# Optimization experiments

Measured on AMD Instinct MI355X. Metric: run time of the kernel, lower is better.

Reference implementation:

```python
import jax, jax.numpy as jnp
import numpy as np

N_NODES = 100000
N_EDGES = 1600000
D = 128


def _sage_conv(x, src, dst, W_l, b_l, W_r, num_nodes):
    # gather source-node features along edges, mean-aggregate at destination
    msg_sum = jax.ops.segment_sum(x[src], dst, num_segments=num_nodes)  # [N, D]
    cnt = jax.ops.segment_sum(jnp.ones((src.shape[0], 1), x.dtype), dst,
                              num_segments=num_nodes)                   # [N, 1]
    agg = msg_sum / jnp.maximum(cnt, 1.0)
    # PyG SAGEConv: lin_l(aggregated) + bias + lin_r(self), root linear has no bias
    return agg @ W_l + b_l + x @ W_r


def setup_inputs() -> dict:
    key = jax.random.key(0)
    ks = jax.random.split(key, 8)
    scale = 1.0 / np.sqrt(D)
    x = jax.random.normal(ks[0], (N_NODES, D), dtype=jnp.float32)
    edge_index = jax.random.randint(ks[1], (2, N_EDGES), 0, N_NODES, dtype=jnp.int64)
    W_l1 = jax.random.normal(ks[2], (D, D), dtype=jnp.float32) * scale
    b_l1 = jnp.zeros((D,), dtype=jnp.float32)
    W_r1 = jax.random.normal(ks[3], (D, D), dtype=jnp.float32) * scale
    W_l2 = jax.random.normal(ks[4], (D, D), dtype=jnp.float32) * scale
    b_l2 = jnp.zeros((D,), dtype=jnp.float32)
    W_r2 = jax.random.normal(ks[5], (D, D), dtype=jnp.float32) * scale
    return {"x": x, "edge_index": edge_index, "W_l1": W_l1, "b_l1": b_l1,
            "W_r1": W_r1, "W_l2": W_l2, "b_l2": b_l2, "W_r2": W_r2}


def reference(x, edge_index, W_l1, b_l1, W_r1, W_l2, b_l2, W_r2):
    src, dst = edge_index[0], edge_index[1]
    n = x.shape[0]
    h = jax.nn.relu(_sage_conv(x, src, dst, W_l1, b_l1, W_r1, n))
    out = _sage_conv(h, src, dst, W_l2, b_l2, W_r2, n)
    return out
```

## Files before the change

kernel.cpp:

```cpp
#include <hip/hip_runtime.h>
#include <hip/hip_bf16.h>

#define DF 128
#define BSH 7
#define BNODES (1 << BSH)
#define SRCBITS 17
#define SRCMASK ((1u << SRCBITS) - 1u)
#define NBLK 512
#define SLABSH 13
#define NKEYS (BNODES * 16)

typedef __attribute__((ext_vector_type(8))) short short8;
typedef __attribute__((ext_vector_type(4))) float floatx4;

__device__ __forceinline__ unsigned short f2bf(float f) {
  unsigned u = __float_as_uint(f);
  u += 0x7fffu + ((u >> 16) & 1u);
  return (unsigned short)(u >> 16);
}
__device__ __forceinline__ float bflo(unsigned u) { return __uint_as_float(u << 16); }
__device__ __forceinline__ float bfhi(unsigned u) { return __uint_as_float(u & 0xffff0000u); }


__global__ __launch_bounds__(256) void count_and_conv(const int* __restrict__ dst,
                                                      int* __restrict__ histg,
                                                      int e, int nb, int chunk,
                                                      const float* __restrict__ x,
                                                      unsigned short* __restrict__ xb, int n4) {
  int t = threadIdx.x;
  if (blockIdx.x < NBLK) {
    __shared__ int h[1024];
    int blk = blockIdx.x;
    for (int i = t; i < nb; i += 256) h[i] = 0;
    __syncthreads();
    int s = blk * chunk, en = min(e, s + chunk);
    for (int i = s + t; i < en; i += 256) atomicAdd(&h[dst[i] >> BSH], 1);
    __syncthreads();
    for (int b = t; b < nb; b += 256) histg[blk * nb + b] = h[b];
  } else {
    int i = (blockIdx.x - NBLK) * 256 + t;
    if (i < n4) {
      float4 v = ((const float4*)x)[i];
      union { unsigned short u[4]; uint2 d; } o;
      o.u[0] = f2bf(v.x); o.u[1] = f2bf(v.y); o.u[2] = f2bf(v.z); o.u[3] = f2bf(v.w);
      ((uint2*)xb)[i] = o.d;
    }
  }
}

__global__ __launch_bounds__(256) void scan_and_reorder(int* __restrict__ histg,
                                                        int* __restrict__ tot, int nb, int sb,
                                                        const float* __restrict__ W0,
                                                        const float* __restrict__ W1,
                                                        const float* __restrict__ W2,
                                                        const float* __restrict__ W3,
                                                        unsigned short* __restrict__ wf) {
  if ((int)blockIdx.x < sb) {
    int wave = threadIdx.x >> 6, lane = threadIdx.x & 63;
    int b = blockIdx.x * 4 + wave;
    if (b >= nb) return;
    int v[8];
    int s = 0;
#pragma unroll
    for (int j = 0; j < 8; ++j) {
      v[j] = histg[(lane * 8 + j) * nb + b];
      s += v[j];
    }
    int S = s;
#pragma unroll
    for (int o = 1; o < 64; o <<= 1) {
      int u = __shfl_up(S, o);
      if (lane >= o) S += u;
    }
    int base = S - s;
#pragma unroll
    for (int j = 0; j < 8; ++j) {
      int c = v[j];
      histg[(lane * 8 + j) * nb + b] = base;
      base += c;
    }
    if (lane == 63) tot[b] = S;
  } else {
    int bb = blockIdx.x - sb;
    int m = bb >> 6;
    const float* W = (m == 0) ? W0 : (m == 1) ? W1 : (m == 2) ? W2 : W3;
    int t = (bb & 63) * 256 + threadIdx.x;
    int j = t & 7, lane = (t >> 3) & 63, ktnt = t >> 9;
    int nt = ktnt & 7, kt = ktnt >> 3;
    int k = kt * 32 + (lane >> 4) * 8 + j;
    int ncol = nt * 16 + (lane & 15);
    wf[m * 16384 + t] = f2bf(W[k * DF + ncol]);
  }
}

__global__ __launch_bounds__(1024) void scan_tot(const int* __restrict__ tot,
                                                 int* __restrict__ bko, int nb, int e) {
  __shared__ int wsum[16];
  int t = threadIdx.x;
  int v = (t < nb) ? tot[t] : 0;
  int lane = t & 63, wid = t >> 6;
  int s = v;
#pragma unroll
  for (int off = 1; off < 64; off <<= 1) {
    int u = __shfl_up(s, off);
    if (lane >= off) s += u;
  }
  if (lane == 63) wsum[wid] = s;
  __syncthreads();
  if (wid == 0) {
    int ws = (lane < 16) ? wsum[lane] : 0;
#pragma unroll
    for (int off = 1; off < 16; off <<= 1) {
      int u = __shfl_up(ws, off);
      if (lane >= off) ws += u;
    }
    if (lane < 16) wsum[lane] = ws;
  }
  __syncthreads();
  int incl = s + ((wid > 0) ? wsum[wid - 1] : 0);
  if (t < nb) bko[t] = incl - v;
  if (t == 0) bko[nb] = e;
}

__global__ __launch_bounds__(256) void part_scatter(const int* __restrict__ src,
                                                    const int* __restrict__ dst,
                                                    const int* __restrict__ histg,
                                                    const int* __restrict__ bko,
                                                    unsigned* __restrict__ ebuf,
                                                    int e, int nb, int chunk) {
  __shared__ int cur[1024];
  int t = threadIdx.x, blk = blockIdx.x;
  for (int b = t; b < nb; b += 256) cur[b] = bko[b] + histg[blk * nb + b];
  __syncthreads();
  int s = blk * chunk, en = min(e, s + chunk);
  for (int i = s + t; i < en; i += 256) {
    int d = dst[i];
    int p = atomicAdd(&cur[d >> BSH], 1);
    ebuf[p] = ((unsigned)(d & (BNODES - 1)) << SRCBITS) | (unsigned)src[i];
  }
}

__global__ __launch_bounds__(256) void fill_fine(const unsigned* __restrict__ ebuf,
                                                 const int* __restrict__ bko,
                                                 int* __restrict__ rs,
                                                 int* __restrict__ csr, int n) {
  __shared__ int hist[NKEYS];
  __shared__ int cur[NKEYS];
  __shared__ int wsum[4];
  int b = blockIdx.x;
  int t = threadIdx.x;
  for (int i = t; i < NKEYS; i += 256) hist[i] = 0;
  __syncthreads();
  int s = bko[b], e = bko[b + 1];
  for (int i = s + t; i < e; i += 256) {
    unsigned p = ebuf[i];
    int key = (int)((p >> SRCBITS) << 4) | (int)((p & SRCMASK) >> SLABSH);
    atomicAdd(&hist[key], 1);
  }
  __syncthreads();
  int v[8], sum = 0;
#pragma unroll
  for (int j = 0; j < 8; ++j) { v[j] = hist[t * 8 + j]; sum += v[j]; }
  int lane = t & 63, wid = t >> 6;
  int S = sum;
#pragma unroll
  for (int o = 1; o < 64; o <<= 1) {
    int u = __shfl_up(S, o);
    if (lane >= o) S += u;
  }
  if (lane == 63) wsum[wid] = S;
  __syncthreads();
  if (wid == 0 && lane < 4) {
    int ws = wsum[lane];
#pragma unroll
    for (int o = 1; o < 4; o <<= 1) {
      int u = __shfl_up(ws, o);
      if (lane >= o) ws += u;
    }
    wsum[lane] = ws;
  }
  __syncthreads();
  int base = (S - sum) + ((wid > 0) ? wsum[wid - 1] : 0);
#pragma unroll
  for (int j = 0; j < 8; ++j) { cur[t * 8 + j] = base; base += v[j]; }
  __syncthreads();
  if (t < BNODES) {
    int g = (b << BSH) + t;
    if (g < n) {
      int endoff = (t == BNODES - 1) ? (e - s) : cur[(t + 1) << 4];
      rs[g] = s + endoff;
    }
  }
  __syncthreads();
  for (int i = s + t; i < e; i += 256) {
    unsigned p = ebuf[i];
    int key = (int)((p >> SRCBITS) << 4) | (int)((p & SRCMASK) >> SLABSH);
    int r = atomicAdd(&cur[key], 1);
    csr[s + r] = (int)(p & SRCMASK);
  }
}

__global__ __launch_bounds__(256) void agg_pull(const uint4* __restrict__ feat,
                                                const int* __restrict__ rs,
                                                const int* __restrict__ csr,
                                                uint4* __restrict__ out, int n) {
  int node = (blockIdx.x * 256 + threadIdx.x) >> 4;
  int l = threadIdx.x & 15;
  if (node >= n) return;
  int s = (node > 0) ? rs[node - 1] : 0;
  int e = rs[node];
  float a0 = 0.f, a1 = 0.f, a2 = 0.f, a3 = 0.f;
  float a4 = 0.f, a5 = 0.f, a6 = 0.f, a7 = 0.f;
  int i = s;
  for (; i + 7 < e; i += 8) {
    int idx[8];
#pragma unroll
    for (int k = 0; k < 8; ++k) idx[k] = csr[i + k];
    uint4 u[8];
#pragma unroll
    for (int k = 0; k < 8; ++k) u[k] = feat[idx[k] * 16 + l];
#pragma unroll
    for (int k = 0; k < 8; ++k) {
      a0 += bflo(u[k].x); a1 += bfhi(u[k].x);
      a2 += bflo(u[k].y); a3 += bfhi(u[k].y);
      a4 += bflo(u[k].z); a5 += bfhi(u[k].z);
      a6 += bflo(u[k].w); a7 += bfhi(u[k].w);
    }
  }
  for (; i < e; ++i) {
    uint4 u = feat[csr[i] * 16 + l];
    a0 += bflo(u.x); a1 += bfhi(u.x);
    a2 += bflo(u.y); a3 += bfhi(u.y);
    a4 += bflo(u.z); a5 += bfhi(u.z);
    a6 += bflo(u.w); a7 += bfhi(u.w);
  }
  float sc = 1.0f / (float)max(e - s, 1);
  uint4 o;
  o.x = (unsigned)f2bf(a0 * sc) | ((unsigned)f2bf(a1 * sc) << 16);
  o.y = (unsigned)f2bf(a2 * sc) | ((unsigned)f2bf(a3 * sc) << 16);
  o.z = (unsigned)f2bf(a4 * sc) | ((unsigned)f2bf(a5 * sc) << 16);
  o.w = (unsigned)f2bf(a6 * sc) | ((unsigned)f2bf(a7 * sc) << 16);
  out[node * 16 + l] = o;
}

__global__ __launch_bounds__(256) void gemm_sage(const unsigned short* __restrict__ Aagg,
                                                 const unsigned short* __restrict__ Aself,
                                                 const unsigned short* __restrict__ WFl,
                                                 const unsigned short* __restrict__ WFr,
                                                 const float* __restrict__ bias,
                                                 void* __restrict__ outp, int n,
                                                 int relu_out_bf16) {
  int wave = threadIdx.x >> 6;
  int lane = threadIdx.x & 63;
  int l16 = lane & 15, quad = lane >> 4;
  int rbase = (blockIdx.x * 4 + wave) * 32;
  if (rbase >= n) return;

  floatx4 acc[2][8];
#pragma unroll
  for (int a = 0; a < 2; ++a)
#pragma unroll
    for (int b = 0; b < 8; ++b) acc[a][b] = (floatx4)0.0f;

  int r0 = min(rbase + l16, n - 1);
  int r1 = min(rbase + 16 + l16, n - 1);

#pragma unroll
  for (int s = 0; s < 2; ++s) {
    const unsigned short* A = s ? Aself : Aagg;
    const unsigned short* W = s ? WFr : WFl;
#pragma unroll
    for (int kt = 0; kt < 4; ++kt) {
      short8 a0 = *(const short8*)(A + r0 * DF + kt * 32 + quad * 8);
      short8 a1 = *(const short8*)(A + r1 * DF + kt * 32 + quad * 8);
#pragma unroll
      for (int nt = 0; nt < 8; ++nt) {
        short8 bf = *(const short8*)(W + (((kt * 8 + nt) * 64) + lane) * 8);
        acc[0][nt] = __builtin_amdgcn_mfma_f32_16x16x32_bf16(a0, bf, acc[0][nt], 0, 0, 0);
        acc[1][nt] = __builtin_amdgcn_mfma_f32_16x16x32_bf16(a1, bf, acc[1][nt], 0, 0, 0);
      }
    }
  }

  float bv[8];
#pragma unroll
  for (int nt = 0; nt < 8; ++nt) bv[nt] = bias[nt * 16 + l16];

  if (relu_out_bf16) {
    unsigned short* O = (unsigned short*)outp;
#pragma unroll
    for (int rb = 0; rb < 2; ++rb)
#pragma unroll
      for (int i = 0; i < 4; ++i) {
        int row = rbase + rb * 16 + quad * 4 + i;
        if (row < n) {
#pragma unroll
          for (int nt = 0; nt < 8; ++nt) {
            float v = acc[rb][nt][i] + bv[nt];
            O[row * DF + nt * 16 + l16] = f2bf(fmaxf(v, 0.0f));
          }
        }
      }
  } else {
    float* O = (float*)outp;
#pragma unroll
    for (int rb = 0; rb < 2; ++rb)
#pragma unroll
      for (int i = 0; i < 4; ++i) {
        int row = rbase + rb * 16 + quad * 4 + i;
        if (row < n) {
#pragma unroll
          for (int nt = 0; nt < 8; ++nt)
            O[row * DF + nt * 16 + l16] = acc[rb][nt][i] + bv[nt];
        }
      }
  }
}


extern "C" void kernel_launch(void* const* d_in, const int* in_sizes, int n_in,
                              void* d_out, int out_size, void* d_ws, size_t ws_size,
                              hipStream_t stream) {
  const float* x   = (const float*)d_in[0];
  const int*   ei  = (const int*)d_in[1];
  const float* Wl1 = (const float*)d_in[2];
  const float* bl1 = (const float*)d_in[3];
  const float* Wr1 = (const float*)d_in[4];
  const float* Wl2 = (const float*)d_in[5];
  const float* bl2 = (const float*)d_in[6];
  const float* Wr2 = (const float*)d_in[7];

  int n = in_sizes[0] / DF;
  int e = in_sizes[1] / 2;
  const int* srcv = ei;
  const int* dstv = ei + e;
  int nb = (n + BNODES - 1) >> BSH;
  int chunk = (e + NBLK - 1) / NBLK;

  char* ws = (char*)d_ws;
  size_t off = 0;
  auto alloc = [&](size_t bytes) {
    void* p = ws + off;
    off = (off + bytes + 255) & ~(size_t)255;
    return p;
  };
  int* histg = (int*)alloc((size_t)nb * NBLK * 4);
  int* tot   = (int*)alloc(4096);
  int* bko   = (int*)alloc((size_t)(nb + 1) * 4);
  int* rs    = (int*)alloc((size_t)n * 4);
  unsigned* ebuf = (unsigned*)alloc((size_t)e * 4);
  int* csr   = (int*)alloc((size_t)e * 4);
  unsigned short* xb   = (unsigned short*)alloc((size_t)n * DF * 2);
  unsigned short* hb   = (unsigned short*)alloc((size_t)n * DF * 2);
  unsigned short* aggb = (unsigned short*)alloc((size_t)n * DF * 2);
  unsigned short* wf   = (unsigned short*)alloc(4 * DF * DF * 2);
  unsigned short* wfl1 = wf;
  unsigned short* wfr1 = wf + 16384;
  unsigned short* wfl2 = wf + 32768;
  unsigned short* wfr2 = wf + 49152;

  int n4 = n * DF / 4;
  int cb = (n4 + 255) / 256;
  count_and_conv<<<NBLK + cb, 256, 0, stream>>>(dstv, histg, e, nb, chunk, x, xb, n4);
  int sb = (nb + 3) / 4;
  scan_and_reorder<<<sb + 256, 256, 0, stream>>>(histg, tot, nb, sb,
                                                 Wl1, Wr1, Wl2, Wr2, wf);
  scan_tot<<<1, 1024, 0, stream>>>(tot, bko, nb, e);
  part_scatter<<<NBLK, 256, 0, stream>>>(srcv, dstv, histg, bko, ebuf, e, nb, chunk);
  fill_fine<<<nb, 256, 0, stream>>>(ebuf, bko, rs, csr, n);

  agg_pull<<<(n * 16 + 255) / 256, 256, 0, stream>>>((const uint4*)xb, rs, csr,
                                                     (uint4*)aggb, n);
  gemm_sage<<<(n + 127) / 128, 256, 0, stream>>>(aggb, xb, wfl1, wfr1, bl1, hb, n, 1);
  agg_pull<<<(n * 16 + 255) / 256, 256, 0, stream>>>((const uint4*)hb, rs, csr,
                                                     (uint4*)aggb, n);
  gemm_sage<<<(n + 127) / 128, 256, 0, stream>>>(aggb, hb, wfl2, wfr2, bl2, d_out, n, 0);
}
```

Measured before the change: 361.5 us.

## Fuse neighbor mean-aggregation into SAGE GEMM via swizzled shared-memory tile

Merges the gather/mean aggregation kernel and the MFMA GEMM into one kernel per layer. Each block aggregates 128 nodes into an XOR-swizzled LDS tile, then multiplies that tile by W_l and the self features by W_r. This removes the bf16 aggregate buffer's global write and re-read plus two launches. In exchange each block now does 8 sequential node aggregations per 16-lane group, and the grid shrinks to about 782 blocks, which may lower memory-level parallelism for the latency-bound gather.

```diff
diff --git a/kernel.cpp b/kernel.cpp
--- a/kernel.cpp
+++ b/kernel.cpp
@@ -48,6 +48,7 @@
   }
 }
 
+
 __global__ __launch_bounds__(256) void scan_and_reorder(int* __restrict__ histg,
                                                         int* __restrict__ tot, int nb, int sb,
                                                         const float* __restrict__ W0,
@@ -200,85 +201,102 @@
   }
 }
 
-__global__ __launch_bounds__(256) void agg_pull(const uint4* __restrict__ feat,
-                                                const int* __restrict__ rs,
-                                                const int* __restrict__ csr,
-                                                uint4* __restrict__ out, int n) {
-  int node = (blockIdx.x * 256 + threadIdx.x) >> 4;
-  int l = threadIdx.x & 15;
-  if (node >= n) return;
-  int s = (node > 0) ? rs[node - 1] : 0;
-  int e = rs[node];
-  float a0 = 0.f, a1 = 0.f, a2 = 0.f, a3 = 0.f;
-  float a4 = 0.f, a5 = 0.f, a6 = 0.f, a7 = 0.f;
-  int i = s;
-  for (; i + 7 < e; i += 8) {
-    int idx[8];
-#pragma unroll
-    for (int k = 0; k < 8; ++k) idx[k] = csr[i + k];
-    uint4 u[8];
-#pragma unroll
-    for (int k = 0; k < 8; ++k) u[k] = feat[idx[k] * 16 + l];
-#pragma unroll
-    for (int k = 0; k < 8; ++k) {
-      a0 += bflo(u[k].x); a1 += bfhi(u[k].x);
-      a2 += bflo(u[k].y); a3 += bfhi(u[k].y);
-      a4 += bflo(u[k].z); a5 += bfhi(u[k].z);
-      a6 += bflo(u[k].w); a7 += bfhi(u[k].w);
-    }
-  }
-  for (; i < e; ++i) {
-    uint4 u = feat[csr[i] * 16 + l];
-    a0 += bflo(u.x); a1 += bfhi(u.x);
-    a2 += bflo(u.y); a3 += bfhi(u.y);
-    a4 += bflo(u.z); a5 += bfhi(u.z);
-    a6 += bflo(u.w); a7 += bfhi(u.w);
-  }
-  float sc = 1.0f / (float)max(e - s, 1);
-  uint4 o;
-  o.x = (unsigned)f2bf(a0 * sc) | ((unsigned)f2bf(a1 * sc) << 16);
-  o.y = (unsigned)f2bf(a2 * sc) | ((unsigned)f2bf(a3 * sc) << 16);
-  o.z = (unsigned)f2bf(a4 * sc) | ((unsigned)f2bf(a5 * sc) << 16);
-  o.w = (unsigned)f2bf(a6 * sc) | ((unsigned)f2bf(a7 * sc) << 16);
-  out[node * 16 + l] = o;
-}
-
-__global__ __launch_bounds__(256) void gemm_sage(const unsigned short* __restrict__ Aagg,
-                                                 const unsigned short* __restrict__ Aself,
-                                                 const unsigned short* __restrict__ WFl,
-                                                 const unsigned short* __restrict__ WFr,
-                                                 const float* __restrict__ bias,
-                                                 void* __restrict__ outp, int n,
-                                                 int relu_out_bf16) {
-  int wave = threadIdx.x >> 6;
-  int lane = threadIdx.x & 63;
+__global__ __launch_bounds__(256) void sage_fused(const uint4* __restrict__ feat,
+                                                  const int* __restrict__ rs,
+                                                  const int* __restrict__ csr,
+                                                  const unsigned short* __restrict__ WFl,
+                                                  const unsigned short* __restrict__ WFr,
+                                                  const float* __restrict__ bias,
+                                                  void* __restrict__ outp, int n,
+                                                  int relu_out_bf16) {
+  __shared__ uint4 As[BNODES][16];
+  int t = threadIdx.x;
+  int b = blockIdx.x;
+  int g = t >> 4, l = t & 15;
+
+  for (int j = 0; j < 8; ++j) {
+    int lr = g * 8 + j;
+    int node = (b << BSH) + lr;
+    uint4 o;
+    if (node < n) {
+      int s = (node > 0) ? rs[node - 1] : 0;
+      int e = rs[node];
+      float a0 = 0.f, a1 = 0.f, a2 = 0.f, a3 = 0.f;
+      float a4 = 0.f, a5 = 0.f, a6 = 0.f, a7 = 0.f;
+      int i = s;
+      for (; i + 7 < e; i += 8) {
+        int idx[8];
+#pragma unroll
+        for (int k = 0; k < 8; ++k) idx[k] = csr[i + k];
+        uint4 u[8];
+#pragma unroll
+        for (int k = 0; k < 8; ++k) u[k] = feat[idx[k] * 16 + l];
+#pragma unroll
+        for (int k = 0; k < 8; ++k) {
+          a0 += bflo(u[k].x); a1 += bfhi(u[k].x);
+          a2 += bflo(u[k].y); a3 += bfhi(u[k].y);
+          a4 += bflo(u[k].z); a5 += bfhi(u[k].z);
+          a6 += bflo(u[k].w); a7 += bfhi(u[k].w);
+        }
+      }
+      for (; i < e; ++i) {
+        uint4 u = feat[csr[i] * 16 + l];
+        a0 += bflo(u.x); a1 += bfhi(u.x);
+        a2 += bflo(u.y); a3 += bfhi(u.y);
+        a4 += bflo(u.z); a5 += bfhi(u.z);
+        a6 += bflo(u.w); a7 += bfhi(u.w);
+      }
+      float sc = 1.0f / (float)max(e - s, 1);
+      o.x = (unsigned)f2bf(a0 * sc) | ((unsigned)f2bf(a1 * sc) << 16);
+      o.y = (unsigned)f2bf(a2 * sc) | ((unsigned)f2bf(a3 * sc) << 16);
+      o.z = (unsigned)f2bf(a4 * sc) | ((unsigned)f2bf(a5 * sc) << 16);
+      o.w = (unsigned)f2bf(a6 * sc) | ((unsigned)f2bf(a7 * sc) << 16);
+    } else {
+      o.x = 0u; o.y = 0u; o.z = 0u; o.w = 0u;
+    }
+    As[lr][l ^ (lr & 7)] = o;
+  }
+  __syncthreads();
+
+  int wave = t >> 6;
+  int lane = t & 63;
   int l16 = lane & 15, quad = lane >> 4;
-  int rbase = (blockIdx.x * 4 + wave) * 32;
-  if (rbase >= n) return;
+  int rbase = wave * 32;
+  int grow = (b << BSH) + rbase;
+  if (grow >= n) return;
 
   floatx4 acc[2][8];
 #pragma unroll
   for (int a = 0; a < 2; ++a)
 #pragma unroll
-    for (int b = 0; b < 8; ++b) acc[a][b] = (floatx4)0.0f;
-
-  int r0 = min(rbase + l16, n - 1);
-  int r1 = min(rbase + 16 + l16, n - 1);
-
-#pragma unroll
-  for (int s = 0; s < 2; ++s) {
-    const unsigned short* A = s ? Aself : Aagg;
-    const unsigned short* W = s ? WFr : WFl;
-#pragma unroll
-    for (int kt = 0; kt < 4; ++kt) {
-      short8 a0 = *(const short8*)(A + r0 * DF + kt * 32 + quad * 8);
-      short8 a1 = *(const short8*)(A + r1 * DF + kt * 32 + quad * 8);
-#pragma unroll
-      for (int nt = 0; nt < 8; ++nt) {
-        short8 bf = *(const short8*)(W + (((kt * 8 + nt) * 64) + lane) * 8);
-        acc[0][nt] = __builtin_amdgcn_mfma_f32_16x16x32_bf16(a0, bf, acc[0][nt], 0, 0, 0);
-        acc[1][nt] = __builtin_amdgcn_mfma_f32_16x16x32_bf16(a1, bf, acc[1][nt], 0, 0, 0);
-      }
+    for (int c = 0; c < 8; ++c) acc[a][c] = (floatx4)0.0f;
+
+  int r0l = rbase + l16;
+  int r1l = rbase + 16 + l16;
+  const unsigned short* Asf = (const unsigned short*)feat;
+  int r0g = min(grow + l16, n - 1);
+  int r1g = min(grow + 16 + l16, n - 1);
+
+#pragma unroll
+  for (int kt = 0; kt < 4; ++kt) {
+    short8 a0 = *(const short8*)&As[r0l][(kt * 4 + quad) ^ (r0l & 7)];
+    short8 a1 = *(const short8*)&As[r1l][(kt * 4 + quad) ^ (r1l & 7)];
+#pragma unroll
+    for (int nt = 0; nt < 8; ++nt) {
+      short8 bf = *(const short8*)(WFl + (((kt * 8 + nt) * 64) + lane) * 8);
+      acc[0][nt] = __builtin_amdgcn_mfma_f32_16x16x32_bf16(a0, bf, acc[0][nt], 0, 0, 0);
+      acc[1][nt] = __builtin_amdgcn_mfma_f32_16x16x32_bf16(a1, bf, acc[1][nt], 0, 0, 0);
+    }
+  }
+#pragma unroll
+  for (int kt = 0; kt < 4; ++kt) {
+    short8 a0 = *(const short8*)(Asf + r0g * DF + kt * 32 + quad * 8);
+    short8 a1 = *(const short8*)(Asf + r1g * DF + kt * 32 + quad * 8);
+#pragma unroll
+    for (int nt = 0; nt < 8; ++nt) {
+      short8 bf = *(const short8*)(WFr + (((kt * 8 + nt) * 64) + lane) * 8);
+      acc[0][nt] = __builtin_amdgcn_mfma_f32_16x16x32_bf16(a0, bf, acc[0][nt], 0, 0, 0);
+      acc[1][nt] = __builtin_amdgcn_mfma_f32_16x16x32_bf16(a1, bf, acc[1][nt], 0, 0, 0);
     }
   }
 
@@ -292,7 +310,7 @@
     for (int rb = 0; rb < 2; ++rb)
 #pragma unroll
       for (int i = 0; i < 4; ++i) {
-        int row = rbase + rb * 16 + quad * 4 + i;
+        int row = grow + rb * 16 + quad * 4 + i;
         if (row < n) {
 #pragma unroll
           for (int nt = 0; nt < 8; ++nt) {
@@ -307,7 +325,7 @@
     for (int rb = 0; rb < 2; ++rb)
 #pragma unroll
       for (int i = 0; i < 4; ++i) {
-        int row = rbase + rb * 16 + quad * 4 + i;
+        int row = grow + rb * 16 + quad * 4 + i;
         if (row < n) {
 #pragma unroll
           for (int nt = 0; nt < 8; ++nt)
@@ -352,7 +370,6 @@
   int* csr   = (int*)alloc((size_t)e * 4);
   unsigned short* xb   = (unsigned short*)alloc((size_t)n * DF * 2);
   unsigned short* hb   = (unsigned short*)alloc((size_t)n * DF * 2);
-  unsigned short* aggb = (unsigned short*)alloc((size_t)n * DF * 2);
   unsigned short* wf   = (unsigned short*)alloc(4 * DF * DF * 2);
   unsigned short* wfl1 = wf;
   unsigned short* wfr1 = wf + 16384;
@@ -369,10 +386,6 @@
   part_scatter<<<NBLK, 256, 0, stream>>>(srcv, dstv, histg, bko, ebuf, e, nb, chunk);
   fill_fine<<<nb, 256, 0, stream>>>(ebuf, bko, rs, csr, n);
 
-  agg_pull<<<(n * 16 + 255) / 256, 256, 0, stream>>>((const uint4*)xb, rs, csr,
-                                                     (uint4*)aggb, n);
-  gemm_sage<<<(n + 127) / 128, 256, 0, stream>>>(aggb, xb, wfl1, wfr1, bl1, hb, n, 1);
-  agg_pull<<<(n * 16 + 255) / 256, 256, 0, stream>>>((const uint4*)hb, rs, csr,
-                                                     (uint4*)aggb, n);
-  gemm_sage<<<(n + 127) / 128, 256, 0, stream>>>(aggb, hb, wfl2, wfr2, bl2, d_out, n, 0);
-}
+  sage_fused<<<nb, 256, 0, stream>>>((const uint4*)xb, rs, csr, wfl1, wfr1, bl1, hb, n, 1);
+  sage_fused<<<nb, 256, 0, stream>>>((const uint4*)hb, rs, csr, wfl2, wfr2, bl2, d_out, n, 0);
+}
```

After: 420.1 us. +16.2%, slower.
